# Performance work log

Measured on AMD Instinct MI355X. Metric: run time of the kernel, lower is better.

## Reference

```python
import jax, jax.numpy as jnp
import numpy as np

B, C, H, W = 16, 1536, 32, 32
M = 64      # num_clusters
L = 128     # cluster_dim
G = 256     # token_dim
HID = 512
OT_ITERS = 3
EPS = 1e-6


def setup_inputs() -> dict:
    key = jax.random.key(0)
    ks = jax.random.split(key, 12)
    def w(k, shape, fan_in):
        return jax.random.normal(k, shape, jnp.float32) * (1.0 / np.sqrt(fan_in))
    return {
        'x': jax.random.normal(ks[0], (B, C, H, W), jnp.float32),
        't': jax.random.normal(ks[1], (B, C), jnp.float32),
        # token_features: Linear(C->512), ReLU, Linear(512->G)
        'Wt1': w(ks[2], (HID, C), C), 'bt1': jnp.zeros((HID,), jnp.float32),
        'Wt2': w(ks[3], (G, HID), HID), 'bt2': jnp.zeros((G,), jnp.float32),
        # cluster_features: 1x1 Conv(C->512), ReLU, 1x1 Conv(512->L)
        'Wc1': w(ks[4], (HID, C), C), 'bc1': jnp.zeros((HID,), jnp.float32),
        'Wc2': w(ks[5], (L, HID), HID), 'bc2': jnp.zeros((L,), jnp.float32),
        # score: 1x1 Conv(C->512), ReLU, 1x1 Conv(512->M)
        'Ws1': w(ks[6], (HID, C), C), 'bs1': jnp.zeros((HID,), jnp.float32),
        'Ws2': w(ks[7], (M, HID), HID), 'bs2': jnp.zeros((M,), jnp.float32),
        # temp_predictor: Conv1d(L->1, k=1)
        'Wtp': w(ks[8], (L,), L), 'btp': jnp.zeros((), jnp.float32),
        'dust_bin': jnp.asarray(1.0, jnp.float32),
        'burst_b': jnp.asarray(0.0, jnp.float32),
        'burst_p': jnp.asarray(1.0, jnp.float32),
        'lambda_discount': jnp.asarray(0.5, jnp.float32),
    }


def _log_optimal_transport(scores, alpha, iters):
    # scores: [B, m, n]; alpha: scalar dust-bin logit
    b, m, n = scores.shape
    Z0 = jnp.concatenate([scores, jnp.broadcast_to(alpha, (b, 1, n))], axis=1)  # [B, m+1, n]
    norm = -jnp.log(jnp.asarray(m + n, scores.dtype))
    log_mu = jnp.concatenate([jnp.full((m,), norm, scores.dtype),
                              (jnp.log(jnp.asarray(n, scores.dtype)) + norm)[None]])  # [m+1]
    log_nu = jnp.full((n,), norm, scores.dtype)
    u = jnp.zeros((b, m + 1), scores.dtype)
    v = jnp.zeros((b, n), scores.dtype)
    for _ in range(iters):
        u = log_mu - jax.nn.logsumexp(Z0 + v[:, None, :], axis=2)
        v = log_nu - jax.nn.logsumexp(Z0 + u[:, :, None], axis=1)
    return Z0 + u[:, :, None] + v[:, None, :] - norm


def _l2norm(a, axis):
    return a / jnp.maximum(jnp.linalg.norm(a, axis=axis, keepdims=True), 1e-12)


def _forward(x, t, Wt1, bt1, Wt2, bt2, Wc1, bc1, Wc2, bc2, Ws1, bs1, Ws2, bs2,
             Wtp, btp, dust_bin, burst_b, burst_p, lambda_discount):
    b, c, h, w = x.shape
    n = h * w
    xf = x.reshape(b, c, n)  # [B, C, N] (1x1 convs == per-pixel MLP)
    # cluster features f: [B, L, N]
    h1 = jax.nn.relu(jnp.einsum('bcn,oc->bon', xf, Wc1) + bc1[:, None])
    f = jnp.einsum('bhn,lh->bln', h1, Wc2) + bc2[:, None]
    # assignment scores p: [B, M, N]
    h2 = jax.nn.relu(jnp.einsum('bcn,oc->bon', xf, Ws1) + bs1[:, None])
    p = jnp.einsum('bhn,mh->bmn', h2, Ws2) + bs2[:, None]
    # global token: [B, G]
    tok = jax.nn.relu(t @ Wt1.T + bt1) @ Wt2.T + bt2
    # Sinkhorn OT soft assignment, drop dust bin row
    P = jnp.exp(_log_optimal_transport(p, dust_bin, OT_ITERS))[:, :-1, :]  # [B, M, N]
    # burst-aware weighting
    f_norm = _l2norm(f, axis=1)                                  # [B, L, N]
    T_i = jax.nn.softplus(jnp.einsum('bln,l->bn', f, Wtp) + btp)  # [B, N]
    sim = jnp.einsum('bli,blj->bij', f_norm, f_norm)              # [B, N, N]
    T_avg = (T_i[:, :, None] + T_i[:, None, :]) * 0.5
    burst_w = jax.nn.sigmoid(T_avg * sim + burst_b)
    discount = jnp.clip(jnp.sum(burst_w, axis=-1) ** burst_p, 1e-3, 1e3)  # [B, N]
    lam = jax.nn.sigmoid(lambda_discount)
    P_adj = (1.0 - lam) * P + lam * (P / (discount[:, None, :] + EPS))
    # local aggregation: (f[:, :, None, :] * P[:, None, :, :]).sum(-1) == batched matmul
    agg = jnp.einsum('bln,bmn->blm', f, P_adj)  # [B, L, M]
    agg = _l2norm(agg, axis=1).reshape(b, -1)   # [B, L*M]
    tok_n = _l2norm(tok, axis=-1)
    g = jnp.concatenate([tok_n, agg], axis=-1)  # [B, G + L*M]
    return _l2norm(g, axis=-1)


def reference(x, t, Wt1, bt1, Wt2, bt2, Wc1, bc1, Wc2, bc2, Ws1, bs1, Ws2, bs2,
              Wtp, btp, dust_bin, burst_b, burst_p, lambda_discount):
    return _forward(x, t, Wt1, bt1, Wt2, bt2, Wc1, bc1, Wc2, bc2, Ws1, bs1, Ws2, bs2,
                    Wtp, btp, dust_bin, burst_b, burst_p, lambda_discount)
```

## Files before the change

### kernel.cpp

```cpp
#include <hip/hip_runtime.h>
#include <math.h>

#define B_   16
#define C_   1536
#define N_   1024
#define M_   64
#define L_   128
#define G_   256
#define HID_ 512

typedef __attribute__((ext_vector_type(8))) short short8;
typedef __attribute__((ext_vector_type(4))) float floatx4;

__device__ __forceinline__ unsigned short f2bf_rne(float x) {
    unsigned u = __float_as_uint(x);
    unsigned r = u + 0x7fffu + ((u >> 16) & 1u);
    return (unsigned short)(r >> 16);
}
__device__ __forceinline__ unsigned pack_bf2(float lo, float hi) {
    unsigned a = __float_as_uint(lo) + 0x8000u;
    unsigned b = __float_as_uint(hi) + 0x8000u;
    return (a >> 16) | (b & 0xffff0000u);
}

__device__ __forceinline__ void gl2lds16(const void* g, void* l) {
    __builtin_amdgcn_global_load_lds(
        (const __attribute__((address_space(1))) void*)g,
        (__attribute__((address_space(3))) void*)l, 16, 0, 0);
}

__global__ __launch_bounds__(256) void cast_w_kernel(
    const float* __restrict__ Wc1, const float* __restrict__ Ws1,
    const float* __restrict__ Wc2, const float* __restrict__ Ws2,
    unsigned short* __restrict__ Wbf, unsigned short* __restrict__ W2)
{
    const int V1 = 393216;
    const int VH = 196608;
    int idx = blockIdx.x * 256 + threadIdx.x;
    if (idx < V1) {
        const float4* src = (idx < VH) ? (const float4*)Wc1 : (const float4*)Ws1;
        float4 v = src[(idx < VH) ? idx : idx - VH];
        ushort4 o;
        o.x = f2bf_rne(v.x); o.y = f2bf_rne(v.y);
        o.z = f2bf_rne(v.z); o.w = f2bf_rne(v.w);
        ((ushort4*)Wbf)[idx] = o;
    } else if (idx < V1 + 192 * 1024) {
        int i2 = idx - V1;
        int row = i2 >> 10, k = i2 & 1023;
        float v = 0.f;
        if (row < 128) { if (k < 512) v = Wc2[row * 512 + k]; }
        else           { if (k >= 512) v = Ws2[(row - 128) * 512 + (k - 512)]; }
        W2[i2] = f2bf_rne(v);
    }
}

__global__ __launch_bounds__(256) void xt_kernel(
    const float* __restrict__ x, unsigned short* __restrict__ xT)
{
    __shared__ float Xs[64][65];
    const int t = threadIdx.x;
    const int n0 = blockIdx.x * 64, c0 = blockIdx.y * 64, b = blockIdx.z;
    const float* xb = x + (long)b * C_ * N_;
    #pragma unroll
    for (int it = 0; it < 16; ++it) {
        int idx = it * 256 + t, cr = idx >> 6, nc = idx & 63;
        Xs[cr][nc] = xb[(long)(c0 + cr) * N_ + n0 + nc];
    }
    __syncthreads();
    unsigned* xo = (unsigned*)(xT + (long)b * N_ * C_);
    #pragma unroll
    for (int it = 0; it < 8; ++it) {
        int idx = it * 256 + t, nr = idx >> 5, pc = idx & 31;
        xo[(long)(n0 + nr) * 768 + (c0 >> 1) + pc] =
            pack_bf2(Xs[2 * pc][nr], Xs[2 * pc + 1][nr]);
    }
}

#define G1_STAGE_A(kt, q)                                                    \
    gl2lds16(aSrc + (long)(q) * (32 * C_) + (kt) * 64,                       \
             (char*)g1lds + (((kt) & 1) * 65536 + (q) * 8192) + sdst)
#define G1_STAGE_B(kt, q)                                                    \
    gl2lds16(bSrc + (long)(q) * (32 * C_) + (kt) * 64,                       \
             (char*)g1lds + (((kt) & 1) * 65536 + 32768 + (q) * 8192) + sdst)

#define G1_PHASE(q, STAGES, TAIL)                                            \
  {                                                                          \
    const char* ab = cb + aFB + (q) * 8192;                                  \
    short8 a0 = *(const short8*)(ab + ks0);                                  \
    short8 a1 = *(const short8*)(ab + ks1);                                  \
    short8 a2 = *(const short8*)(ab + 2048 + ks0);                           \
    short8 a3 = *(const short8*)(ab + 2048 + ks1);                           \
    STAGES                                                                   \
    __builtin_amdgcn_s_barrier();                                            \
    asm volatile("s_waitcnt lgkmcnt(0)" ::: "memory");                       \
    __builtin_amdgcn_sched_barrier(0);                                       \
    __builtin_amdgcn_s_setprio(1);                                           \
    _Pragma("unroll")                                                        \
    for (int fj = 0; fj < 4; ++fj) {                                         \
      acc[2*(q)][fj]   = __builtin_amdgcn_mfma_f32_16x16x32_bf16(            \
          a0, bfr[fj][0], acc[2*(q)][fj], 0, 0, 0);                          \
      acc[2*(q)][fj]   = __builtin_amdgcn_mfma_f32_16x16x32_bf16(            \
          a1, bfr[fj][1], acc[2*(q)][fj], 0, 0, 0);                          \
      acc[2*(q)+1][fj] = __builtin_amdgcn_mfma_f32_16x16x32_bf16(            \
          a2, bfr[fj][0], acc[2*(q)+1][fj], 0, 0, 0);                        \
      acc[2*(q)+1][fj] = __builtin_amdgcn_mfma_f32_16x16x32_bf16(            \
          a3, bfr[fj][1], acc[2*(q)+1][fj], 0, 0, 0);                        \
    }                                                                        \
    __builtin_amdgcn_s_setprio(0);                                           \
    TAIL                                                                     \
    __builtin_amdgcn_s_barrier();                                            \
    __builtin_amdgcn_sched_barrier(0);                                       \
  }

#define G1_TILE(tt, S1, S2, TAIL3)                                           \
  {                                                                          \
    const char* cb = (const char*)g1lds + ((tt) & 1) * 65536;                \
    _Pragma("unroll")                                                        \
    for (int fj = 0; fj < 4; ++fj) {                                         \
      const char* bb = cb + bFB + (fj >> 1) * 8192 + (fj & 1) * 2048;        \
      bfr[fj][0] = *(const short8*)(bb + ks0);                               \
      bfr[fj][1] = *(const short8*)(bb + ks1);                               \
    }                                                                        \
    G1_PHASE(0, if (S1) { G1_STAGE_A((tt)+1, 2); G1_STAGE_A((tt)+1, 3); }, ) \
    G1_PHASE(1, if (S2) { G1_STAGE_B((tt)+2, 0); G1_STAGE_B((tt)+2, 1); }, ) \
    G1_PHASE(2, if (S2) { G1_STAGE_B((tt)+2, 2); G1_STAGE_B((tt)+2, 3); }, ) \
    G1_PHASE(3, if (S2) { G1_STAGE_A((tt)+2, 0); G1_STAGE_A((tt)+2, 1); }, TAIL3) \
  }

__global__ __launch_bounds__(512, 2) void gemm1_kernel(
    const unsigned short* __restrict__ Wbf, const unsigned short* __restrict__ xT,
    const float* __restrict__ bc1, const float* __restrict__ bs1,
    unsigned short* __restrict__ hT)
{
    __shared__ unsigned short g1lds[65536];
    const int t = threadIdx.x;
    const int lane = t & 63, w = t >> 6;
    const int f = blockIdx.x + (blockIdx.y << 2) + (blockIdx.z << 4);
    const int g = ((f & 7) << 5) + (f >> 3);
    const int n0 = (g & 3) * 256, o0 = ((g >> 2) & 3) * 256, b = g >> 4;

    const int sgrow = ((t & 256) ? 128 : 0) + ((t >> 3) & 31);
    const int sdst  = t * 16;
    const int sslot = ((t & 7) ^ ((t >> 3) & 7)) * 8;
    const unsigned short* aSrc = Wbf + (long)(o0 + sgrow) * C_ + sslot;
    const unsigned short* bSrc = xT + (long)b * N_ * C_
                               + (long)(n0 + sgrow) * C_ + sslot;

    const int lrow = lane & 15, kgrp = lane >> 4;
    const int wo = (w >> 2) * 128, wn = (w & 3) * 64;
    const int aFB = (w >> 2) * 4096 + lrow * 128;
    const int bFB = 32768 + ((w >> 1) & 1) * 4096 + (w & 1) * 16384 + lrow * 128;
    const int ks0 = (kgrp ^ (lrow & 7)) * 16;
    const int ks1 = ((4 + kgrp) ^ (lrow & 7)) * 16;

    floatx4 acc[8][4];
    #pragma unroll
    for (int i = 0; i < 8; ++i)
        #pragma unroll
        for (int j = 0; j < 4; ++j) acc[i][j] = (floatx4)0.0f;
    short8 bfr[4][2];

    #pragma unroll
    for (int q = 0; q < 4; ++q) { G1_STAGE_A(0, q); G1_STAGE_B(0, q); }
    #pragma unroll
    for (int q = 0; q < 4; ++q) G1_STAGE_B(1, q);
    G1_STAGE_A(1, 0); G1_STAGE_A(1, 1);
    asm volatile("s_waitcnt vmcnt(6)" ::: "memory");
    __builtin_amdgcn_s_barrier();
    __builtin_amdgcn_sched_barrier(0);

    #pragma unroll 2
    for (int t8 = 0; t8 < 22; ++t8)
        G1_TILE(t8, 1, 1, asm volatile("s_waitcnt vmcnt(6)" ::: "memory");)
    G1_TILE(22, 1, 0, asm volatile("s_waitcnt vmcnt(0)" ::: "memory");)
    G1_TILE(23, 0, 0, )

    const float* bias = (o0 < 512) ? bc1 : bs1;
    const int ob = (o0 < 512) ? o0 : o0 - 512;
    #pragma unroll
    for (int fi = 0; fi < 8; ++fi) {
        const int orow = wo + fi * 16 + kgrp * 4;
        float4 bv = *(const float4*)&bias[ob + orow];
        #pragma unroll
        for (int fj = 0; fj < 4; ++fj) {
            const int n = n0 + wn + fj * 16 + lrow;
            float v0 = fmaxf(acc[fi][fj][0] + bv.x, 0.f);
            float v1 = fmaxf(acc[fi][fj][1] + bv.y, 0.f);
            float v2 = fmaxf(acc[fi][fj][2] + bv.z, 0.f);
            float v3 = fmaxf(acc[fi][fj][3] + bv.w, 0.f);
            uint2 pk;
            pk.x = ((unsigned)f2bf_rne(v0)) | (((unsigned)f2bf_rne(v1)) << 16);
            pk.y = ((unsigned)f2bf_rne(v2)) | (((unsigned)f2bf_rne(v3)) << 16);
            *(uint2*)&hT[((long)b * N_ + n) * 1024 + o0 + orow] = pk;
        }
    }
}

__global__ __launch_bounds__(256, 2) void gemm23_kernel(
    const unsigned short* __restrict__ W2, const unsigned short* __restrict__ hT,
    const float* __restrict__ bc2, const float* __restrict__ bs2,
    float* __restrict__ f, float* __restrict__ p)
{
    __shared__ unsigned short As[64 * 32];
    __shared__ unsigned short Bs[128 * 32];
    const int t = threadIdx.x;
    const int lane = t & 63, w = t >> 6;
    const int n0 = blockIdx.x * 128, o0 = blockIdx.y * 64, b = blockIdx.z;
    const unsigned short* hTb = hT + (long)b * N_ * 1024;

    const int wo = (w >> 1) * 32, wn = (w & 1) * 64;
    const int lrow = lane & 15, kgrp = lane >> 4;
    const int arow = t >> 2, acol = (t & 3) * 8;
    const int klo = (o0 < 128) ? 0 : 512;

    floatx4 acc[2][4];
    #pragma unroll
    for (int i = 0; i < 2; ++i)
        #pragma unroll
        for (int j = 0; j < 4; ++j) acc[i][j] = (floatx4)0.0f;

    for (int k0 = 0; k0 < 512; k0 += 32) {
        gl2lds16(W2 + (long)(o0 + arow) * 1024 + klo + k0 + acol, (char*)As + t * 16);
        #pragma unroll
        for (int r = 0; r < 2; ++r)
            gl2lds16(hTb + (long)(n0 + r * 64 + arow) * 1024 + klo + k0 + acol,
                     (char*)Bs + r * 4096 + t * 16);
        __syncthreads();
        short8 af[2], bfr[4];
        #pragma unroll
        for (int i = 0; i < 2; ++i)
            af[i] = *(const short8*)((const char*)As +
                        (wo + i * 16 + lrow) * 64 + kgrp * 16);
        #pragma unroll
        for (int j = 0; j < 4; ++j)
            bfr[j] = *(const short8*)((const char*)Bs +
                        (wn + j * 16 + lrow) * 64 + kgrp * 16);
        #pragma unroll
        for (int i = 0; i < 2; ++i)
            #pragma unroll
            for (int j = 0; j < 4; ++j)
                acc[i][j] = __builtin_amdgcn_mfma_f32_16x16x32_bf16(
                    af[i], bfr[j], acc[i][j], 0, 0, 0);
        __syncthreads();
    }

    #pragma unroll
    for (int i = 0; i < 2; ++i) {
        int o = o0 + wo + i * 16 + kgrp * 4;
        #pragma unroll
        for (int j = 0; j < 4; ++j) {
            int n = n0 + wn + j * 16 + lrow;
            #pragma unroll
            for (int r = 0; r < 4; ++r) {
                int oo = o + r;
                float v = acc[i][j][r];
                if (oo < 128) f[((long)b * L_ + oo) * N_ + n] = v + bc2[oo];
                else p[((long)b * M_ + (oo - 128)) * N_ + n] = v + bs2[oo - 128];
            }
        }
    }
}

__global__ __launch_bounds__(256) void token1_kernel(
    const float* __restrict__ t_in, const float* __restrict__ Wt1,
    const float* __restrict__ bt1, float* __restrict__ hid)
{
    const int lane = threadIdx.x & 63, w = threadIdx.x >> 6;
    const int o = blockIdx.x * 4 + w, b = blockIdx.y;
    const float4* wr = (const float4*)(Wt1 + (long)o * C_);
    const float4* tb = (const float4*)(t_in + (long)b * C_);
    float acc = 0.f;
    #pragma unroll
    for (int i = 0; i < 6; ++i) {
        float4 a = wr[i * 64 + lane], tv = tb[i * 64 + lane];
        acc += a.x * tv.x + a.y * tv.y + a.z * tv.z + a.w * tv.w;
    }
    #pragma unroll
    for (int off = 1; off < 64; off <<= 1) acc += __shfl_xor(acc, off);
    if (lane == 0) hid[b * HID_ + o] = fmaxf(acc + bt1[o], 0.f);
}

__global__ __launch_bounds__(256) void token2_kernel(
    const float* __restrict__ hid, const float* __restrict__ Wt2,
    const float* __restrict__ bt2, float* __restrict__ tok)
{
    const int lane = threadIdx.x & 63, w = threadIdx.x >> 6;
    const int g = blockIdx.x * 4 + w, b = blockIdx.y;
    const float4* wr = (const float4*)(Wt2 + (long)g * HID_);
    const float4* hb = (const float4*)(hid + (long)b * HID_);
    float acc = 0.f;
    #pragma unroll
    for (int i = 0; i < 2; ++i) {
        float4 a = wr[i * 64 + lane], hv = hb[i * 64 + lane];
        acc += a.x * hv.x + a.y * hv.y + a.z * hv.z + a.w * hv.w;
    }
    #pragma unroll
    for (int off = 1; off < 64; off <<= 1) acc += __shfl_xor(acc, off);
    if (lane == 0) tok[b * G_ + g] = acc + bt2[g];
}

__global__ __launch_bounds__(256) void token3_kernel(
    const float* __restrict__ tok, float* __restrict__ tokn)
{
    __shared__ float red[4];
    const int b = blockIdx.x, t = threadIdx.x;
    float v = tok[b * G_ + t];
    float ss = v * v;
    #pragma unroll
    for (int off = 1; off < 64; off <<= 1) ss += __shfl_xor(ss, off);
    if ((t & 63) == 0) red[t >> 6] = ss;
    __syncthreads();
    float inv = 1.f / fmaxf(sqrtf(red[0] + red[1] + red[2] + red[3]), 1e-12f);
    tokn[b * G_ + t] = v * inv;
}

__global__ __launch_bounds__(256) void ku_first_kernel(
    float* __restrict__ p, const float* __restrict__ dust,
    float* __restrict__ avec)
{
    const int t = threadIdx.x, lane = t & 63, w = t >> 6;
    const int m = blockIdx.x * 4 + w, b = blockIdx.y;
    if (m > M_) return;
    float s = 0.f;
    if (m < M_) {
        float* row = p + ((long)b * M_ + m) * N_;
        #pragma unroll
        for (int i = 0; i < 16; ++i) {
            int n = i * 64 + lane;
            float K = expf(row[n]);
            row[n] = K;
            s += K;
        }
    } else {
        s = 16.f * expf(dust[0]);
    }
    #pragma unroll
    for (int off = 1; off < 64; off <<= 1) s += __shfl_xor(s, off);
    if (lane == 0) {
        float mu = (m < M_) ? (1.f / 1088.f) : (1024.f / 1088.f);
        avec[b * (M_ + 1) + m] = mu / s;
    }
}

__global__ __launch_bounds__(256) void kvku_kernel(
    const float* __restrict__ K, const float* __restrict__ dust,
    const float* __restrict__ avec_in, float* __restrict__ avec_out)
{
    __shared__ float a_s[M_ + 1];
    __shared__ float b_lds[N_];
    const int t = threadIdx.x, lane = t & 63, w = t >> 6;
    const int mg = blockIdx.x, b = blockIdx.y;
    const float ea = expf(dust[0]);
    const float* Kb = K + (long)b * M_ * N_;

    if (t < M_ + 1) a_s[t] = avec_in[b * (M_ + 1) + t];
    __syncthreads();

    #pragma unroll
    for (int k = 0; k < 4; ++k) {
        int n = k * 256 + t;
        float s = ea * a_s[M_];
        const float* col = Kb + n;
        #pragma unroll
        for (int m = 0; m < M_; ++m) s = fmaf(col[(long)m * N_], a_s[m], s);
        b_lds[n] = (1.f / 1088.f) / s;
    }
    __syncthreads();

    const int m = mg * 4 + w;
    if (m > M_) return;
    float s = 0.f;
    if (m < M_) {
        const float* row = Kb + (long)m * N_;
        #pragma unroll
        for (int i = 0; i < 16; ++i) {
            int n = i * 64 + lane;
            s = fmaf(row[n], b_lds[n], s);
        }
    } else {
        #pragma unroll
        for (int i = 0; i < 16; ++i) s += b_lds[i * 64 + lane];
        s *= ea;
    }
    #pragma unroll
    for (int off = 1; off < 64; off <<= 1) s += __shfl_xor(s, off);
    if (lane == 0) {
        float mu = (m < M_) ? (1.f / 1088.f) : (1024.f / 1088.f);
        avec_out[b * (M_ + 1) + m] = mu / s;
    }
}

__global__ __launch_bounds__(256) void tnorm_kernel(
    const float* __restrict__ f, const float* __restrict__ Wtp,
    const float* __restrict__ btp, unsigned short* __restrict__ fnT,
    float* __restrict__ T, float* __restrict__ draw, float* __restrict__ aggz)
{
    __shared__ float Ft[L_][65];
    __shared__ float red_ss[4][64];
    __shared__ float red_dot[4][64];
    __shared__ float invs[64];
    __shared__ float wtp_s[L_];
    const int b = blockIdx.y, n0 = blockIdx.x * 64, t = threadIdx.x;
    const float* fb = f + (long)b * L_ * N_;

    if (t < L_) wtp_s[t] = Wtp[t];
    for (int it = 0; it < 32; ++it) {
        int idx = it * 256 + t;
        int l = idx >> 6, c = idx & 63;
        Ft[l][c] = fb[(long)l * N_ + n0 + c];
    }
    __syncthreads();
    {
        const int lg = t >> 6, col = t & 63;
        float ss = 0.f, dot = 0.f;
        #pragma unroll
        for (int i = 0; i < 32; ++i) {
            int l = lg * 32 + i;
            float v = Ft[l][col];
            ss = fmaf(v, v, ss);
            dot = fmaf(v, wtp_s[l], dot);
        }
        red_ss[lg][col] = ss;
        red_dot[lg][col] = dot;
    }
    {
        int base = (b * 16 + blockIdx.x) * 512;
        aggz[base + t] = 0.f;
        aggz[base + 256 + t] = 0.f;
    }
    __syncthreads();
    if (t < 64) {
        float ss = ((red_ss[0][t] + red_ss[1][t]) + (red_ss[2][t] + red_ss[3][t]));
        float dot = ((red_dot[0][t] + red_dot[1][t]) + (red_dot[2][t] + red_dot[3][t]));
        invs[t] = 1.f / fmaxf(sqrtf(ss), 1e-12f);
        float xx = dot + btp[0];
        T[b * N_ + n0 + t] = (xx > 0.f) ? (xx + log1pf(expf(-xx)))
                                        : log1pf(expf(xx));
        draw[b * N_ + n0 + t] = 0.f;
    }
    __syncthreads();
    unsigned* fo = (unsigned*)fnT;
    for (int it = 0; it < 16; ++it) {
        int idx = it * 256 + t;
        int nl = idx >> 6, jp = idx & 63;
        float inv = invs[nl];
        fo[(((long)b * N_ + n0 + nl) << 6) + jp] =
            pack_bf2(Ft[2 * jp][nl] * inv, Ft[2 * jp + 1][nl] * inv);
    }
}

__global__ __launch_bounds__(256) void sim_kernel(
    const unsigned short* __restrict__ fnT, const float* __restrict__ T,
    const float* __restrict__ bb, float* __restrict__ draw)
{
    __shared__ unsigned short As[64 * 136];
    __shared__ unsigned short Bs[64 * 136];
    __shared__ float Ti[64], Tj[64];
    const int b = blockIdx.z, i0 = blockIdx.y * 64, j0base = blockIdx.x * 256;
    const int t = threadIdx.x, lane = t & 63, w = t >> 6;
    const int lrow = lane & 15, kgrp = lane >> 4;
    const unsigned short* fb = fnT + (long)b * N_ * 128;
    const float burstb = bb[0];

    if (t < 64) Ti[t] = T[b * N_ + i0 + t];
    const int srow = t >> 4, scol = (t & 15) * 8;
    #pragma unroll
    for (int r = 0; r < 4; ++r) {
        uint4 av = *(const uint4*)(fb + (long)(i0 + r * 16 + srow) * 128 + scol);
        *(uint4*)((char*)As + (r * 16 + srow) * 272 + scol * 2) = av;
    }
    uint4 bv[4];
    #pragma unroll
    for (int r = 0; r < 4; ++r)
        bv[r] = *(const uint4*)(fb + (long)(j0base + r * 16 + srow) * 128 + scol);

    float rs[4] = {0.f, 0.f, 0.f, 0.f};
    #pragma unroll
    for (int jj = 0; jj < 4; ++jj) {
        __syncthreads();
        #pragma unroll
        for (int r = 0; r < 4; ++r)
            *(uint4*)((char*)Bs + (r * 16 + srow) * 272 + scol * 2) = bv[r];
        if (t >= 64 && t < 128) Tj[t - 64] = T[b * N_ + j0base + jj * 64 + (t - 64)];
        if (jj < 3) {
            #pragma unroll
            for (int r = 0; r < 4; ++r)
                bv[r] = *(const uint4*)(fb +
                    (long)(j0base + (jj + 1) * 64 + r * 16 + srow) * 128 + scol);
        }
        __syncthreads();

        floatx4 acc[4];
        #pragma unroll
        for (int j = 0; j < 4; ++j) acc[j] = (floatx4)0.0f;
        __builtin_amdgcn_s_setprio(1);
        #pragma unroll
        for (int k0 = 0; k0 < 128; k0 += 32) {
            short8 af = *(const short8*)((const char*)As +
                            (w * 16 + lrow) * 272 + k0 * 2 + kgrp * 16);
            #pragma unroll
            for (int j = 0; j < 4; ++j) {
                short8 bf = *(const short8*)((const char*)Bs +
                                (j * 16 + lrow) * 272 + k0 * 2 + kgrp * 16);
                acc[j] = __builtin_amdgcn_mfma_f32_16x16x32_bf16(af, bf, acc[j], 0, 0, 0);
            }
        }
        __builtin_amdgcn_s_setprio(0);
        #pragma unroll
        for (int j = 0; j < 4; ++j) {
            float Tjv = Tj[j * 16 + lrow];
            #pragma unroll
            for (int r = 0; r < 4; ++r) {
                float Tiv = Ti[w * 16 + kgrp * 4 + r];
                float xarg = 0.5f * (Tiv + Tjv) * acc[j][r] + burstb;
                rs[r] += 1.f / (1.f + expf(-xarg));
            }
        }
    }

    #pragma unroll
    for (int off = 1; off < 16; off <<= 1)
        #pragma unroll
        for (int r = 0; r < 4; ++r) rs[r] += __shfl_xor(rs[r], off);
    if (lrow == 0) {
        #pragma unroll
        for (int r = 0; r < 4; ++r)
            atomicAdd(&draw[b * N_ + i0 + w * 16 + kgrp * 4 + r], rs[r]);
    }
}

__global__ __launch_bounds__(256) void agg_kernel(
    const float* __restrict__ f, const float* __restrict__ Kmat,
    const float* __restrict__ avec, const float* __restrict__ dust,
    const float* __restrict__ draw, const float* __restrict__ bp,
    const float* __restrict__ lamd, float* __restrict__ agg)
{
    __shared__ float fch[L_][65];
    __shared__ float Pch[M_][65];
    __shared__ float a_s[M_ + 1], cf[64];
    const int b = blockIdx.y, n0 = blockIdx.x * 64;
    const int t = threadIdx.x, tx = t & 15, ty = t >> 4;
    const float* fb = f + (long)b * L_ * N_;
    const float* Kb = Kmat + (long)b * M_ * N_;

    if (t < M_ + 1) a_s[t] = avec[b * (M_ + 1) + t];
    __syncthreads();

    for (int idx = t; idx < L_ * 64; idx += 256) {
        int l = idx >> 6, c = idx & 63;
        fch[l][c] = fb[(long)l * N_ + n0 + c];
    }
    for (int idx = t; idx < M_ * 64; idx += 256) {
        int m = idx >> 6, c = idx & 63;
        Pch[m][c] = Kb[(long)m * N_ + n0 + c] * a_s[m];
    }
    __syncthreads();

    if (t < 64) {
        float s = expf(dust[0]) * a_s[M_];
        #pragma unroll
        for (int m = 0; m < M_; ++m) s += Pch[m][t];
        float d = powf(draw[b * N_ + n0 + t], bp[0]);
        d = fminf(fmaxf(d, 1e-3f), 1e3f);
        float lam = 1.f / (1.f + expf(-lamd[0]));
        cf[t] = ((1.f - lam) + lam / (d + 1e-6f)) / s;
    }
    __syncthreads();

    float acc[8][4] = {};
    for (int n = 0; n < 64; ++n) {
        float cfn = cf[n];
        float fv[8], pv[4];
        #pragma unroll
        for (int i = 0; i < 8; ++i) fv[i] = fch[ty + 16 * i][n];
        #pragma unroll
        for (int j = 0; j < 4; ++j) pv[j] = Pch[tx * 4 + j][n] * cfn;
        #pragma unroll
        for (int i = 0; i < 8; ++i)
            #pragma unroll
            for (int j = 0; j < 4; ++j)
                acc[i][j] = fmaf(fv[i], pv[j], acc[i][j]);
    }
    #pragma unroll
    for (int i = 0; i < 8; ++i)
        #pragma unroll
        for (int j = 0; j < 4; ++j)
            atomicAdd(&agg[((long)b * L_ + (ty + 16 * i)) * M_ + tx * 4 + j],
                      acc[i][j]);
}

__global__ __launch_bounds__(256) void final_kernel(
    const float* __restrict__ tokn, const float* __restrict__ agg,
    float* __restrict__ out)
{
    __shared__ float invm[M_];
    __shared__ float red[4];
    __shared__ float s_invtot;
    const int b = blockIdx.x, t = threadIdx.x;
    const float* ab = agg + (long)b * L_ * M_;

    if (t < 64) {
        float ss = 0.f;
        for (int l = 0; l < L_; ++l) {
            float v = ab[l * M_ + t];
            ss = fmaf(v, v, ss);
        }
        invm[t] = 1.f / fmaxf(sqrtf(ss), 1e-12f);
    }
    __syncthreads();

    float part;
    {
        float tn = tokn[b * G_ + t];
        part = tn * tn;
    }
    for (int idx = t; idx < L_ * M_; idx += 256) {
        float v = ab[idx] * invm[idx & 63];
        part = fmaf(v, v, part);
    }
    for (int off = 32; off; off >>= 1) part += __shfl_down(part, off);
    if ((t & 63) == 0) red[t >> 6] = part;
    __syncthreads();
    if (t == 0)
        s_invtot = 1.f / fmaxf(sqrtf(red[0] + red[1] + red[2] + red[3]), 1e-12f);
    __syncthreads();

    const float invtot = s_invtot;
    float* ob = out + (long)b * (G_ + L_ * M_);
    ob[t] = tokn[b * G_ + t] * invtot;
    for (int idx = t; idx < L_ * M_; idx += 256)
        ob[G_ + idx] = ab[idx] * invm[idx & 63] * invtot;
}

extern "C" void kernel_launch(void* const* d_in, const int* in_sizes, int n_in,
                              void* d_out, int out_size, void* d_ws, size_t ws_size,
                              hipStream_t stream)
{
    const float* x    = (const float*)d_in[0];
    const float* t_in = (const float*)d_in[1];
    const float* Wt1  = (const float*)d_in[2];
    const float* bt1  = (const float*)d_in[3];
    const float* Wt2  = (const float*)d_in[4];
    const float* bt2  = (const float*)d_in[5];
    const float* Wc1  = (const float*)d_in[6];
    const float* bc1  = (const float*)d_in[7];
    const float* Wc2  = (const float*)d_in[8];
    const float* bc2  = (const float*)d_in[9];
    const float* Ws1  = (const float*)d_in[10];
    const float* bs1  = (const float*)d_in[11];
    const float* Ws2  = (const float*)d_in[12];
    const float* bs2  = (const float*)d_in[13];
    const float* Wtp  = (const float*)d_in[14];
    const float* btp  = (const float*)d_in[15];
    const float* dust = (const float*)d_in[16];
    const float* bb   = (const float*)d_in[17];
    const float* bp   = (const float*)d_in[18];
    const float* lamd = (const float*)d_in[19];

    char* wsb = (char*)d_ws;
    unsigned short* xT  = (unsigned short*)wsb;
    float* f    = (float*)(wsb + 0);
    float* p    = (float*)(wsb + 8388608);
    unsigned short* fnT = (unsigned short*)(wsb + 12582912);
    float* hid  = (float*)(wsb + 16777216);
    float* tok  = (float*)(wsb + 16809984);
    float* tokn = (float*)(wsb + 16826368);
    float* T    = (float*)(wsb + 16842752);
    float* draw = (float*)(wsb + 16908288);
    float* agg  = (float*)(wsb + 17039360);
    float* avec = (float*)(wsb + 17563648);
    float* avec2= (float*)(wsb + 17567808);
    unsigned short* hT  = (unsigned short*)(wsb + 50331648);
    unsigned short* Wbf = (unsigned short*)(wsb + 83886080);
    unsigned short* W2  = (unsigned short*)(wsb + 87031808);
    float* out  = (float*)d_out;

    cast_w_kernel<<<2304, 256, 0, stream>>>(Wc1, Ws1, Wc2, Ws2, Wbf, W2);

    xt_kernel   <<<dim3(16, 24, 16), 256, 0, stream>>>(x, xT);
    gemm1_kernel<<<dim3(4, 4, 16), 512, 0, stream>>>(Wbf, xT, bc1, bs1, hT);
    gemm23_kernel<<<dim3(8, 3, 16), 256, 0, stream>>>(W2, hT, bc2, bs2, f, p);

    token1_kernel<<<dim3(128, 16), 256, 0, stream>>>(t_in, Wt1, bt1, hid);
    token2_kernel<<<dim3(64, 16), 256, 0, stream>>>(hid, Wt2, bt2, tok);
    token3_kernel<<<16, 256, 0, stream>>>(tok, tokn);

    ku_first_kernel<<<dim3(17, 16), 256, 0, stream>>>(p, dust, avec);
    kvku_kernel    <<<dim3(17, 16), 256, 0, stream>>>(p, dust, avec, avec2);
    kvku_kernel    <<<dim3(17, 16), 256, 0, stream>>>(p, dust, avec2, avec);

    tnorm_kernel<<<dim3(16, 16), 256, 0, stream>>>(f, Wtp, btp, fnT, T, draw, agg);
    sim_kernel  <<<dim3(4, 16, 16), 256, 0, stream>>>(fnT, T, bb, draw);
    agg_kernel  <<<dim3(16, 16), 256, 0, stream>>>(f, p, avec, dust, draw, bp, lamd, agg);
    final_kernel<<<16, 256, 0, stream>>>(tokn, agg, out);
}
```

Measured before the change: 391.9 us.

## Vectorize transpose, drop gemm1 block swizzle, replace agg atomics with partial sums

The x transpose kernel now loads with float4 and stores packed bf16 in 8-byte chunks, so it issues fewer and wider memory operations. gemm1 loses its block-index swizzle and maps blocks directly to tiles, which may change L2 locality. The aggregation kernel writes per-chunk partial results to a workspace buffer instead of doing global float atomics, and the final kernel sums the 16 partials in shared memory. This also removes the zero-initialisation of the accumulator in tnorm, at the cost of more workspace traffic in the final kernel.

```diff
diff --git a/kernel.cpp b/kernel.cpp
--- a/kernel.cpp
+++ b/kernel.cpp
@@ -62,17 +62,23 @@
     const int n0 = blockIdx.x * 64, c0 = blockIdx.y * 64, b = blockIdx.z;
     const float* xb = x + (long)b * C_ * N_;
     #pragma unroll
-    for (int it = 0; it < 16; ++it) {
-        int idx = it * 256 + t, cr = idx >> 6, nc = idx & 63;
-        Xs[cr][nc] = xb[(long)(c0 + cr) * N_ + n0 + nc];
-    }
-    __syncthreads();
-    unsigned* xo = (unsigned*)(xT + (long)b * N_ * C_);
-    #pragma unroll
-    for (int it = 0; it < 8; ++it) {
-        int idx = it * 256 + t, nr = idx >> 5, pc = idx & 31;
-        xo[(long)(n0 + nr) * 768 + (c0 >> 1) + pc] =
-            pack_bf2(Xs[2 * pc][nr], Xs[2 * pc + 1][nr]);
+    for (int it = 0; it < 4; ++it) {
+        int idx = it * 256 + t, cr = idx >> 4, fc = idx & 15;
+        float4 v = *(const float4*)&xb[(long)(c0 + cr) * N_ + n0 + fc * 4];
+        Xs[cr][fc * 4 + 0] = v.x;
+        Xs[cr][fc * 4 + 1] = v.y;
+        Xs[cr][fc * 4 + 2] = v.z;
+        Xs[cr][fc * 4 + 3] = v.w;
+    }
+    __syncthreads();
+    uint2* xo = (uint2*)(xT + (long)b * N_ * C_);
+    #pragma unroll
+    for (int it = 0; it < 4; ++it) {
+        int idx = it * 256 + t, nr = idx >> 4, pc = idx & 15;
+        uint2 o;
+        o.x = pack_bf2(Xs[4 * pc + 0][nr], Xs[4 * pc + 1][nr]);
+        o.y = pack_bf2(Xs[4 * pc + 2][nr], Xs[4 * pc + 3][nr]);
+        xo[(long)(n0 + nr) * 384 + (c0 >> 2) + pc] = o;
     }
 }
 
@@ -135,9 +141,7 @@
     __shared__ unsigned short g1lds[65536];
     const int t = threadIdx.x;
     const int lane = t & 63, w = t >> 6;
-    const int f = blockIdx.x + (blockIdx.y << 2) + (blockIdx.z << 4);
-    const int g = ((f & 7) << 5) + (f >> 3);
-    const int n0 = (g & 3) * 256, o0 = ((g >> 2) & 3) * 256, b = g >> 4;
+    const int n0 = blockIdx.x * 256, o0 = blockIdx.y * 256, b = blockIdx.z;
 
     const int sgrow = ((t & 256) ? 128 : 0) + ((t >> 3) & 31);
     const int sdst  = t * 16;
@@ -393,7 +397,7 @@
 __global__ __launch_bounds__(256) void tnorm_kernel(
     const float* __restrict__ f, const float* __restrict__ Wtp,
     const float* __restrict__ btp, unsigned short* __restrict__ fnT,
-    float* __restrict__ T, float* __restrict__ draw, float* __restrict__ aggz)
+    float* __restrict__ T, float* __restrict__ draw)
 {
     __shared__ float Ft[L_][65];
     __shared__ float red_ss[4][64];
@@ -422,11 +426,6 @@
         }
         red_ss[lg][col] = ss;
         red_dot[lg][col] = dot;
-    }
-    {
-        int base = (b * 16 + blockIdx.x) * 512;
-        aggz[base + t] = 0.f;
-        aggz[base + 256 + t] = 0.f;
     }
     __syncthreads();
     if (t < 64) {
@@ -533,12 +532,12 @@
     const float* __restrict__ f, const float* __restrict__ Kmat,
     const float* __restrict__ avec, const float* __restrict__ dust,
     const float* __restrict__ draw, const float* __restrict__ bp,
-    const float* __restrict__ lamd, float* __restrict__ agg)
+    const float* __restrict__ lamd, float* __restrict__ aggp)
 {
     __shared__ float fch[L_][65];
     __shared__ float Pch[M_][65];
     __shared__ float a_s[M_ + 1], cf[64];
-    const int b = blockIdx.y, n0 = blockIdx.x * 64;
+    const int b = blockIdx.y, nb = blockIdx.x, n0 = nb * 64;
     const int t = threadIdx.x, tx = t & 15, ty = t >> 4;
     const float* fb = f + (long)b * L_ * N_;
     const float* Kb = Kmat + (long)b * M_ * N_;
@@ -581,28 +580,37 @@
             for (int j = 0; j < 4; ++j)
                 acc[i][j] = fmaf(fv[i], pv[j], acc[i][j]);
     }
-    #pragma unroll
-    for (int i = 0; i < 8; ++i)
-        #pragma unroll
-        for (int j = 0; j < 4; ++j)
-            atomicAdd(&agg[((long)b * L_ + (ty + 16 * i)) * M_ + tx * 4 + j],
-                      acc[i][j]);
+    float* op = aggp + ((long)b * 16 + nb) * (L_ * M_);
+    #pragma unroll
+    for (int i = 0; i < 8; ++i) {
+        float4 v = make_float4(acc[i][0], acc[i][1], acc[i][2], acc[i][3]);
+        *(float4*)&op[(ty + 16 * i) * M_ + tx * 4] = v;
+    }
 }
 
 __global__ __launch_bounds__(256) void final_kernel(
-    const float* __restrict__ tokn, const float* __restrict__ agg,
+    const float* __restrict__ tokn, const float* __restrict__ aggp,
     float* __restrict__ out)
 {
+    __shared__ float ar[L_ * M_];
     __shared__ float invm[M_];
     __shared__ float red[4];
     __shared__ float s_invtot;
     const int b = blockIdx.x, t = threadIdx.x;
-    const float* ab = agg + (long)b * L_ * M_;
+    const float* pb = aggp + (long)b * 16 * (L_ * M_);
+
+    for (int idx = t; idx < L_ * M_; idx += 256) {
+        float s = 0.f;
+        #pragma unroll
+        for (int nb = 0; nb < 16; ++nb) s += pb[nb * (L_ * M_) + idx];
+        ar[idx] = s;
+    }
+    __syncthreads();
 
     if (t < 64) {
         float ss = 0.f;
         for (int l = 0; l < L_; ++l) {
-            float v = ab[l * M_ + t];
+            float v = ar[l * M_ + t];
             ss = fmaf(v, v, ss);
         }
         invm[t] = 1.f / fmaxf(sqrtf(ss), 1e-12f);
@@ -615,7 +623,7 @@
         part = tn * tn;
     }
     for (int idx = t; idx < L_ * M_; idx += 256) {
-        float v = ab[idx] * invm[idx & 63];
+        float v = ar[idx] * invm[idx & 63];
         part = fmaf(v, v, part);
     }
     for (int off = 32; off; off >>= 1) part += __shfl_down(part, off);
@@ -629,7 +637,7 @@
     float* ob = out + (long)b * (G_ + L_ * M_);
     ob[t] = tokn[b * G_ + t] * invtot;
     for (int idx = t; idx < L_ * M_; idx += 256)
-        ob[G_ + idx] = ab[idx] * invm[idx & 63] * invtot;
+        ob[G_ + idx] = ar[idx] * invm[idx & 63] * invtot;
 }
 
 extern "C" void kernel_launch(void* const* d_in, const int* in_sizes, int n_in,
@@ -667,12 +675,12 @@
     float* tokn = (float*)(wsb + 16826368);
     float* T    = (float*)(wsb + 16842752);
     float* draw = (float*)(wsb + 16908288);
-    float* agg  = (float*)(wsb + 17039360);
     float* avec = (float*)(wsb + 17563648);
     float* avec2= (float*)(wsb + 17567808);
     unsigned short* hT  = (unsigned short*)(wsb + 50331648);
     unsigned short* Wbf = (unsigned short*)(wsb + 83886080);
     unsigned short* W2  = (unsigned short*)(wsb + 87031808);
+    float* aggp = (float*)(wsb + 87425024);
     float* out  = (float*)d_out;
 
     cast_w_kernel<<<2304, 256, 0, stream>>>(Wc1, Ws1, Wc2, Ws2, Wbf, W2);
@@ -689,8 +697,8 @@
     kvku_kernel    <<<dim3(17, 16), 256, 0, stream>>>(p, dust, avec, avec2);
     kvku_kernel    <<<dim3(17, 16), 256, 0, stream>>>(p, dust, avec2, avec);
 
-    tnorm_kernel<<<dim3(16, 16), 256, 0, stream>>>(f, Wtp, btp, fnT, T, draw, agg);
+    tnorm_kernel<<<dim3(16, 16), 256, 0, stream>>>(f, Wtp, btp, fnT, T, draw);
     sim_kernel  <<<dim3(4, 16, 16), 256, 0, stream>>>(fnT, T, bb, draw);
-    agg_kernel  <<<dim3(16, 16), 256, 0, stream>>>(f, p, avec, dust, draw, bp, lamd, agg);
-    final_kernel<<<16, 256, 0, stream>>>(tokn, agg, out);
-}
+    agg_kernel  <<<dim3(16, 16), 256, 0, stream>>>(f, p, avec, dust, draw, bp, lamd, aggp);
+    final_kernel<<<16, 256, 0, stream>>>(tokn, aggp, out);
+}
```

Result: faster. 371.2 us (-5.3%).
